# Performance work log

Hardware: AMD Instinct MI355X
Metric: run time of the kernel (lower is better)

The kernel has to match this reference:

```python
import jax, jax.numpy as jnp
import numpy as np

N_HEAD = 16
D_HEAD = 64
D_HIDN = 1024
B, S = 2, 2048
MASK_FILL = -1e9


def setup_inputs() -> dict:
    key = jax.random.key(0)
    ks = jax.random.split(key, 8)
    scale = 1.0 / np.sqrt(D_HIDN)
    return {
        "Q": jax.random.normal(ks[0], (B, S, D_HIDN), dtype=jnp.float32),
        "K": jax.random.normal(ks[1], (B, S, D_HIDN), dtype=jnp.float32),
        "V": jax.random.normal(ks[2], (B, S, D_HIDN), dtype=jnp.float32),
        "attn_mask": jnp.zeros((B, S, S), dtype=jnp.bool_),
        "Wq": jax.random.normal(ks[3], (D_HIDN, N_HEAD * D_HEAD), dtype=jnp.float32) * scale,
        "bq": jnp.zeros((N_HEAD * D_HEAD,), dtype=jnp.float32),
        "Wk": jax.random.normal(ks[4], (D_HIDN, N_HEAD * D_HEAD), dtype=jnp.float32) * scale,
        "bk": jnp.zeros((N_HEAD * D_HEAD,), dtype=jnp.float32),
        "Wv": jax.random.normal(ks[5], (D_HIDN, N_HEAD * D_HEAD), dtype=jnp.float32) * scale,
        "bv": jnp.zeros((N_HEAD * D_HEAD,), dtype=jnp.float32),
        "Wo": jax.random.normal(ks[6], (N_HEAD * D_HEAD, D_HIDN), dtype=jnp.float32) * scale,
        "bo": jnp.zeros((D_HIDN,), dtype=jnp.float32),
    }


def reference(Q, K, V, attn_mask, Wq, bq, Wk, bk, Wv, bv, Wo, bo):
    b, s, _ = Q.shape
    # projections -> [B, H, S, d_head]
    def split_heads(x):
        return x.reshape(b, -1, N_HEAD, D_HEAD).transpose(0, 2, 1, 3)
    q = split_heads(Q @ Wq + bq)
    k = split_heads(K @ Wk + bk)
    v = split_heads(V @ Wv + bv)
    # scaled dot-product attention with masked_fill(-1e9)
    scores = jnp.einsum("bhqd,bhkd->bhqk", q, k) / jnp.sqrt(jnp.float32(D_HEAD))
    scores = jnp.where(attn_mask[:, None, :, :], MASK_FILL, scores)
    attn_prob = jax.nn.softmax(scores, axis=-1)  # [B,H,S,S]
    context = jnp.einsum("bhqk,bhkd->bhqd", attn_prob, v)
    context = context.transpose(0, 2, 1, 3).reshape(b, s, N_HEAD * D_HEAD)
    output = context @ Wo + bo  # dropout is identity at eval
    return output, attn_prob
```

## Files before the change

### kernel.cpp

```cpp
#include <hip/hip_runtime.h>

typedef _Float16 f16;
typedef _Float16 f16x8 __attribute__((ext_vector_type(8)));
typedef _Float16 f16x4v __attribute__((ext_vector_type(4)));
typedef float f32x4 __attribute__((ext_vector_type(4)));

#define B_   2
#define S_   2048
#define H_   16
#define DH   64
#define DM   1024
#define BS_  (B_ * S_)

#if __has_builtin(__builtin_amdgcn_exp2f)
#define EXP2(x) __builtin_amdgcn_exp2f(x)
#else
#define EXP2(x) exp2f(x)
#endif

#define SCHED_FENCE() __builtin_amdgcn_sched_barrier(0)

__device__ __forceinline__ void gload16(const void* g, void* l) {
  __builtin_amdgcn_global_load_lds((const __attribute__((address_space(1))) unsigned int*)g,
                                   (__attribute__((address_space(3))) unsigned int*)l, 16, 0, 0);
}

__global__ __launch_bounds__(256) void cvt3(const float* __restrict__ a,
                                            const float* __restrict__ b,
                                            const float* __restrict__ c,
                                            f16* __restrict__ oa,
                                            f16* __restrict__ ob,
                                            f16* __restrict__ oc) {
  int t = blockIdx.y;
  const float* in = t == 0 ? a : (t == 1 ? b : c);
  f16* out = t == 0 ? oa : (t == 1 ? ob : oc);
  int i = (blockIdx.x * 256 + threadIdx.x) * 8;
  float4 x = *(const float4*)(in + i);
  float4 y = *(const float4*)(in + i + 4);
  f16x8 o;
  o[0] = (f16)x.x; o[1] = (f16)x.y; o[2] = (f16)x.z; o[3] = (f16)x.w;
  o[4] = (f16)y.x; o[5] = (f16)y.y; o[6] = (f16)y.z; o[7] = (f16)y.w;
  *(f16x8*)(out + i) = o;
}

__global__ __launch_bounds__(256) void wtrans4(const float* __restrict__ w0, const float* __restrict__ w1,
                                               const float* __restrict__ w2, const float* __restrict__ w3,
                                               f16* __restrict__ t0, f16* __restrict__ t1,
                                               f16* __restrict__ t2, f16* __restrict__ t3) {
  __shared__ float t[64][65];
  int z = blockIdx.z;
  const float* w = z == 0 ? w0 : (z == 1 ? w1 : (z == 2 ? w2 : w3));
  f16* wt = z == 0 ? t0 : (z == 1 ? t1 : (z == 2 ? t2 : t3));
  int r0 = blockIdx.y * 64, c0 = blockIdx.x * 64;
  int tid = threadIdx.x;
  int tr = tid >> 2, seg = tid & 3;
#pragma unroll
  for (int jj = 0; jj < 4; ++jj) {
    float4 v = *(const float4*)(w + (size_t)(r0 + tr) * DM + c0 + seg * 16 + jj * 4);
    t[tr][seg * 16 + jj * 4 + 0] = v.x;
    t[tr][seg * 16 + jj * 4 + 1] = v.y;
    t[tr][seg * 16 + jj * 4 + 2] = v.z;
    t[tr][seg * 16 + jj * 4 + 3] = v.w;
  }
  __syncthreads();
#pragma unroll
  for (int jj = 0; jj < 2; ++jj) {
    f16x8 o;
#pragma unroll
    for (int e = 0; e < 8; ++e) o[e] = (f16)t[seg * 16 + jj * 8 + e][tr];
    *(f16x8*)(wt + (size_t)(c0 + tr) * DM + r0 + seg * 16 + jj * 8) = o;
  }
}

__device__ __forceinline__ void gemm_core(const f16* __restrict__ A,
                                          const f16* __restrict__ Bt,
                                          int m0, int n0,
                                          char (&As)[2][16384], char (&Bs)[2][8192],
                                          f32x4 (&acc)[4][2]) {
  const int tid = threadIdx.x;
  const int lane = tid & 63, wid = tid >> 6;
  const int wr = wid >> 1, wc = wid & 1;
  const int l15 = lane & 15, l4 = lane >> 4;
#pragma unroll
  for (int mi = 0; mi < 4; ++mi)
#pragma unroll
    for (int ni = 0; ni < 2; ++ni) { acc[mi][ni][0]=0.f; acc[mi][ni][1]=0.f; acc[mi][ni][2]=0.f; acc[mi][ni][3]=0.f; }

  auto stage = [&](int buf, int kt) {
#pragma unroll
    for (int j = 0; j < 4; ++j) {
      int L = j * 256 + tid;
      int row = L >> 3, seg = L & 7;
      int so = (seg ^ (row & 7)) << 4;
      gload16((const char*)A + ((size_t)(m0 + row) * DM + kt) * 2 + so,
              As[buf] + j * 4096 + wid * 1024);
    }
#pragma unroll
    for (int j = 0; j < 2; ++j) {
      int L = j * 256 + tid;
      int row = L >> 3, seg = L & 7;
      int so = (seg ^ (row & 7)) << 4;
      gload16((const char*)Bt + ((size_t)(n0 + row) * DM + kt) * 2 + so,
              Bs[buf] + j * 4096 + wid * 1024);
    }
  };

  stage(0, 0);
  __syncthreads();
  for (int t = 0; t < 16; ++t) {
    int cur = t & 1;
    if (t < 15) stage(cur ^ 1, (t + 1) * 64);
#pragma unroll
    for (int kk = 0; kk < 2; ++kk) {
      f16x8 af[4], bf[2];
#pragma unroll
      for (int mi = 0; mi < 4; ++mi) {
        int row = wr * 64 + mi * 16 + l15;
        af[mi] = *(const f16x8*)(As[cur] + row * 128 + ((kk * 64 + l4 * 16) ^ ((row & 7) << 4)));
      }
#pragma unroll
      for (int ni = 0; ni < 2; ++ni) {
        int row = wc * 32 + ni * 16 + l15;
        bf[ni] = *(const f16x8*)(Bs[cur] + row * 128 + ((kk * 64 + l4 * 16) ^ ((row & 7) << 4)));
      }
#pragma unroll
      for (int mi = 0; mi < 4; ++mi)
#pragma unroll
        for (int ni = 0; ni < 2; ++ni)
          acc[mi][ni] = __builtin_amdgcn_mfma_f32_16x16x32_f16(af[mi], bf[ni], acc[mi][ni], 0, 0, 0);
    }
    __syncthreads();
  }
}

struct GemmPtrs { const f16* A; const f16* Bt; const float* bias; f16* outh; };

__global__ __launch_bounds__(256, 3) void gemm_proj(GemmPtrs p0, GemmPtrs p1, GemmPtrs p2,
                                                    f16* __restrict__ vout) {
  __shared__ __attribute__((aligned(16))) char As[2][16384];
  __shared__ __attribute__((aligned(16))) char Bs[2][8192];
  int lin = (blockIdx.z * 16 + blockIdx.y) * 32 + blockIdx.x;
  int swz = (lin & 7) * 192 + (lin >> 3);
  int z = swz >> 9, r = swz & 511;
  int m0 = (r >> 4) * 128, n0 = (r & 15) * 64;
  GemmPtrs g = z == 0 ? p0 : (z == 1 ? p1 : p2);

  f32x4 acc[4][2];
  gemm_core(g.A, g.Bt, m0, n0, As, Bs, acc);

  const int tid = threadIdx.x;
  const int lane = tid & 63, wid = tid >> 6;
  const int wr = wid >> 1, wc = wid & 1;
  const int l15 = lane & 15, l4 = lane >> 4;

  if (z != 2) {
#pragma unroll
    for (int mi = 0; mi < 4; ++mi)
#pragma unroll
      for (int ni = 0; ni < 2; ++ni) {
        int gcol = n0 + wc * 32 + ni * 16 + l15;
        float bv = g.bias[gcol];
#pragma unroll
        for (int rr = 0; rr < 4; ++rr) {
          int grow = m0 + wr * 64 + mi * 16 + l4 * 4 + rr;
          int b = grow >> 11, s = grow & 2047, h = gcol >> 6, d = gcol & 63;
          g.outh[(size_t)((b * H_ + h) * S_ + s) * DH + d] = (f16)(acc[mi][ni][rr] + bv);
        }
      }
  } else {
    f16* T2 = (f16*)&As[0][0];
#pragma unroll
    for (int mi = 0; mi < 4; ++mi)
#pragma unroll
      for (int ni = 0; ni < 2; ++ni) {
        int d = wc * 32 + ni * 16 + l15;
        int sl = wr * 64 + mi * 16 + l4 * 4;
        float bv = g.bias[n0 + d];
        f16x4v pv;
        pv[0] = (f16)(acc[mi][ni][0] + bv);
        pv[1] = (f16)(acc[mi][ni][1] + bv);
        pv[2] = (f16)(acc[mi][ni][2] + bv);
        pv[3] = (f16)(acc[mi][ni][3] + bv);
        *(f16x4v*)(T2 + d * 136 + sl) = pv;
      }
    __syncthreads();
    int d = tid >> 2, sq = tid & 3;
    int b = m0 >> 11, s0 = m0 & 2047, h = n0 >> 6;
    const f16* src = T2 + d * 136 + sq * 32;
    f16* dst = vout + ((size_t)((b * H_ + h) * DH + d)) * S_ + s0 + sq * 32;
#pragma unroll
    for (int j = 0; j < 4; ++j)
      *(f16x8*)(dst + j * 8) = *(const f16x8*)(src + j * 8);
  }
}

__global__ __launch_bounds__(256, 3) void gemm_out(const f16* __restrict__ A,
                                                   const f16* __restrict__ Bt,
                                                   const float* __restrict__ bias,
                                                   float* __restrict__ outf) {
  __shared__ __attribute__((aligned(16))) char As[2][16384];
  __shared__ __attribute__((aligned(16))) char Bs[2][8192];
  int lin = blockIdx.y * 32 + blockIdx.x;
  int swz = (lin & 7) * 64 + (lin >> 3);
  int m0 = (swz >> 4) * 128, n0 = (swz & 15) * 64;

  f32x4 acc[4][2];
  gemm_core(A, Bt, m0, n0, As, Bs, acc);

  const int tid = threadIdx.x;
  const int lane = tid & 63, wid = tid >> 6;
  const int wr = wid >> 1, wc = wid & 1;
  const int l15 = lane & 15, l4 = lane >> 4;
#pragma unroll
  for (int mi = 0; mi < 4; ++mi)
#pragma unroll
    for (int ni = 0; ni < 2; ++ni) {
      int gcol = n0 + wc * 32 + ni * 16 + l15;
      float bv = bias[gcol];
#pragma unroll
      for (int rr = 0; rr < 4; ++rr) {
        int grow = m0 + wr * 64 + mi * 16 + l4 * 4 + rr;
        outf[(size_t)grow * DM + gcol] = acc[mi][ni][rr] + bv;
      }
    }
}

__global__ __launch_bounds__(512, 4) void attn_kernel(const f16* __restrict__ q,
                                                      const f16* __restrict__ k,
                                                      const f16* __restrict__ vt,
                                                      const unsigned char* __restrict__ mask,
                                                      float* __restrict__ pout,
                                                      f16* __restrict__ ctxh) {
  __shared__ __attribute__((aligned(16))) char KV[4][8192];
  __shared__ __attribute__((aligned(16))) float P32[8][16][68];
  const int tid = threadIdx.x;
  const int lane = tid & 63, wid = tid >> 6;
  const int l15 = lane & 15, l4 = lane >> 4;

  int lin = blockIdx.y * 16 + blockIdx.x;
  int swz = (lin & 7) * 64 + (lin >> 3);
  const int bx = swz & 15, bh = swz >> 4;
  const int b = bh >> 4, h = bh & 15;
  const int q0w = bx * 128 + wid * 16;

  const f16* qb = q + (size_t)bh * S_ * DH;
  const char* kbc = (const char*)(k + (size_t)bh * S_ * DH);
  const char* vtbc = (const char*)(vt + (size_t)bh * DH * S_);
  const unsigned char* mb = mask + (size_t)b * S_ * S_;
  float* pb = pout + (size_t)bh * S_ * S_;

  const int srow = tid >> 3, sseg = tid & 7;
  const int soff = (sseg ^ (srow & 7)) << 4;

  auto stageK = [&](int buf, int t) {
    gload16(kbc + (size_t)(t * 64 + srow) * 128 + soff, KV[buf] + wid * 1024);
  };
  auto stageV = [&](int buf, int t) {
    gload16(vtbc + (size_t)srow * (S_ * 2) + (size_t)(t * 64) * 2 + soff, KV[buf] + wid * 1024);
  };

  unsigned mmask = 0;
  {
    const unsigned char* mrow = mb + (size_t)(q0w + (lane >> 2)) * S_ + (lane & 3) * 16;
    unsigned acc_or = 0;
#pragma unroll
    for (int tt = 0; tt < 4; ++tt) {
      uint4 mu[8];
#pragma unroll
      for (int u = 0; u < 8; ++u) mu[u] = *(const uint4*)(mrow + (tt * 8 + u) * 64);
#pragma unroll
      for (int u = 0; u < 8; ++u) acc_or |= mu[u].x | mu[u].y | mu[u].z | mu[u].w;
    }
    if (__any(acc_or != 0)) {
      for (int t = 0; t < 32; ++t) {
        uint4 mu = *(const uint4*)(mrow + t * 64);
        if (__any((mu.x | mu.y | mu.z | mu.w) != 0)) mmask |= 1u << t;
      }
    }
  }

  const f16 qs = (f16)0.18033688f;
  f16x8 aq[2];
#pragma unroll
  for (int hh = 0; hh < 2; ++hh) {
    f16x8 v = *(const f16x8*)(qb + (size_t)(q0w + l15) * DH + hh * 32 + l4 * 8);
#pragma unroll
    for (int j = 0; j < 8; ++j) v[j] = v[j] * qs;
    aq[hh] = v;
  }
  SCHED_FENCE();

  float sm[4] = {0.f, 0.f, 0.f, 0.f};

  stageK(0, 0);
  stageK(1, 1);
  for (int p = 0; p < 16; ++p) {
    asm volatile("s_waitcnt vmcnt(0)" ::: "memory");
    __builtin_amdgcn_s_barrier();
    SCHED_FENCE();
    if (p < 15) { stageK((2 * p + 2) & 3, 2 * p + 2); stageK((2 * p + 3) & 3, 2 * p + 3); }
    SCHED_FENCE();
#pragma unroll
    for (int u = 0; u < 2; ++u) {
      const int t = 2 * p + u;
      const char* Kb = KV[t & 3];
      const int kt = t * 64;
      const int anym = (mmask >> t) & 1;
#pragma unroll
      for (int f = 0; f < 4; ++f) {
        int krow = f * 16 + l15;
        f16x8 bk0 = *(const f16x8*)(Kb + krow * 128 + ((l4 * 16) ^ ((krow & 7) << 4)));
        f16x8 bk1 = *(const f16x8*)(Kb + krow * 128 + ((64 + l4 * 16) ^ ((krow & 7) << 4)));
        f32x4 s; s[0]=0.f; s[1]=0.f; s[2]=0.f; s[3]=0.f;
        __builtin_amdgcn_s_setprio(1);
        s = __builtin_amdgcn_mfma_f32_16x16x32_f16(aq[0], bk0, s, 0, 0, 0);
        s = __builtin_amdgcn_mfma_f32_16x16x32_f16(aq[1], bk1, s, 0, 0, 0);
        __builtin_amdgcn_s_setprio(0);
#pragma unroll
        for (int rr = 0; rr < 4; ++rr) {
          float sv = s[rr];
          if (anym) sv = mb[(size_t)(q0w + l4 * 4 + rr) * S_ + kt + f * 16 + l15] ? -1e9f : sv;
          sm[rr] += EXP2(sv);
        }
      }
    }
  }
#pragma unroll
  for (int d = 1; d < 16; d <<= 1)
#pragma unroll
    for (int rr = 0; rr < 4; ++rr) sm[rr] += __shfl_xor(sm[rr], d);
  float inv[4];
#pragma unroll
  for (int rr = 0; rr < 4; ++rr) inv[rr] = 1.0f / sm[rr];

  f32x4 ctx[4];
#pragma unroll
  for (int dc = 0; dc < 4; ++dc) { ctx[dc][0]=0.f; ctx[dc][1]=0.f; ctx[dc][2]=0.f; ctx[dc][3]=0.f; }

  __builtin_amdgcn_s_barrier();
  stageK(0, 0);
  stageV(2, 0);
  __syncthreads();
  for (int t = 0; t < 32; ++t) {
    const int cur = t & 1;
    const int kt = t * 64;
    if (t < 31) { stageK(cur ^ 1, t + 1); stageV(2 + (cur ^ 1), t + 1); }
    SCHED_FENCE();
    const int anym = (mmask >> t) & 1;

#pragma unroll
    for (int f = 0; f < 4; ++f) {
      int krow = f * 16 + l15;
      f16x8 bk0 = *(const f16x8*)(KV[cur] + krow * 128 + ((l4 * 16) ^ ((krow & 7) << 4)));
      f16x8 bk1 = *(const f16x8*)(KV[cur] + krow * 128 + ((64 + l4 * 16) ^ ((krow & 7) << 4)));
      f32x4 s; s[0]=0.f; s[1]=0.f; s[2]=0.f; s[3]=0.f;
      __builtin_amdgcn_s_setprio(1);
      s = __builtin_amdgcn_mfma_f32_16x16x32_f16(aq[0], bk0, s, 0, 0, 0);
      s = __builtin_amdgcn_mfma_f32_16x16x32_f16(aq[1], bk1, s, 0, 0, 0);
      __builtin_amdgcn_s_setprio(0);
#pragma unroll
      for (int rr = 0; rr < 4; ++rr) {
        float sv = s[rr];
        if (anym) sv = mb[(size_t)(q0w + l4 * 4 + rr) * S_ + kt + f * 16 + l15] ? -1e9f : sv;
        float p = EXP2(sv) * inv[rr];
        P32[wid][l4 * 4 + rr][f * 16 + l15] = p;
      }
    }
#pragma unroll
    for (int j = 0; j < 4; ++j) {
      int row = j * 4 + l4;
      f32x4 v = *(const f32x4*)&P32[wid][row][l15 * 4];
      __builtin_nontemporal_store(v, (f32x4*)(pb + (size_t)(q0w + row) * S_ + kt + l15 * 4));
    }
#pragma unroll
    for (int kk = 0; kk < 2; ++kk) {
      f32x4 x = *(const f32x4*)&P32[wid][l15][kk * 32 + l4 * 8];
      f32x4 y = *(const f32x4*)&P32[wid][l15][kk * 32 + l4 * 8 + 4];
      f16x8 pa;
      pa[0] = (f16)x[0]; pa[1] = (f16)x[1]; pa[2] = (f16)x[2]; pa[3] = (f16)x[3];
      pa[4] = (f16)y[0]; pa[5] = (f16)y[1]; pa[6] = (f16)y[2]; pa[7] = (f16)y[3];
      f16x8 bv0, bv1, bv2, bv3;
      {
        int vr0 = 0 * 16 + l15, vr1 = 1 * 16 + l15, vr2 = 2 * 16 + l15, vr3 = 3 * 16 + l15;
        bv0 = *(const f16x8*)(KV[2 + cur] + vr0 * 128 + ((kk * 64 + l4 * 16) ^ ((vr0 & 7) << 4)));
        bv1 = *(const f16x8*)(KV[2 + cur] + vr1 * 128 + ((kk * 64 + l4 * 16) ^ ((vr1 & 7) << 4)));
        bv2 = *(const f16x8*)(KV[2 + cur] + vr2 * 128 + ((kk * 64 + l4 * 16) ^ ((vr2 & 7) << 4)));
        bv3 = *(const f16x8*)(KV[2 + cur] + vr3 * 128 + ((kk * 64 + l4 * 16) ^ ((vr3 & 7) << 4)));
      }
      __builtin_amdgcn_s_setprio(1);
      ctx[0] = __builtin_amdgcn_mfma_f32_16x16x32_f16(pa, bv0, ctx[0], 0, 0, 0);
      ctx[1] = __builtin_amdgcn_mfma_f32_16x16x32_f16(pa, bv1, ctx[1], 0, 0, 0);
      ctx[2] = __builtin_amdgcn_mfma_f32_16x16x32_f16(pa, bv2, ctx[2], 0, 0, 0);
      ctx[3] = __builtin_amdgcn_mfma_f32_16x16x32_f16(pa, bv3, ctx[3], 0, 0, 0);
      __builtin_amdgcn_s_setprio(0);
    }

    if (t < 31) {
      asm volatile("s_waitcnt vmcnt(4)" ::: "memory");
      __builtin_amdgcn_s_barrier();
      SCHED_FENCE();
    }
  }

#pragma unroll
  for (int dc = 0; dc < 4; ++dc)
#pragma unroll
    for (int rr = 0; rr < 4; ++rr)
      ctxh[(size_t)(b * S_ + q0w + l4 * 4 + rr) * DM + h * DH + dc * 16 + l15] = (f16)ctx[dc][rr];
}

extern "C" void kernel_launch(void* const* d_in, const int* in_sizes, int n_in,
                              void* d_out, int out_size, void* d_ws, size_t ws_size,
                              hipStream_t stream) {
  (void)in_sizes; (void)n_in; (void)out_size; (void)ws_size;
  const float* Q  = (const float*)d_in[0];
  const float* K  = (const float*)d_in[1];
  const float* V  = (const float*)d_in[2];
  const unsigned char* mask = (const unsigned char*)d_in[3];
  const float* Wq = (const float*)d_in[4];
  const float* bq = (const float*)d_in[5];
  const float* Wk = (const float*)d_in[6];
  const float* bk = (const float*)d_in[7];
  const float* Wv = (const float*)d_in[8];
  const float* bv = (const float*)d_in[9];
  const float* Wo = (const float*)d_in[10];
  const float* bo = (const float*)d_in[11];

  f16* ws = (f16*)d_ws;
  f16* Xq  = ws;
  f16* Xk  = Xq + 4194304;
  f16* Xv  = Xk + 4194304;
  f16* Wqt = Xv + 4194304;
  f16* Wkt = Wqt + 1048576;
  f16* Wvt = Wkt + 1048576;
  f16* Wot = Wvt + 1048576;
  f16* qh  = Wot + 1048576;
  f16* kh  = qh + 4194304;
  f16* vth = kh + 4194304;
  f16* ctx = Xq;

  float* out0 = (float*)d_out;
  float* pout = out0 + (size_t)BS_ * DM;

  cvt3<<<dim3(2048, 3), dim3(256), 0, stream>>>(Q, K, V, Xq, Xk, Xv);
  wtrans4<<<dim3(16, 16, 4), dim3(256), 0, stream>>>(Wq, Wk, Wv, Wo, Wqt, Wkt, Wvt, Wot);

  GemmPtrs pq{Xq, Wqt, bq, qh};
  GemmPtrs pk{Xk, Wkt, bk, kh};
  GemmPtrs pv{Xv, Wvt, bv, nullptr};
  gemm_proj<<<dim3(32, 16, 3), dim3(256), 0, stream>>>(pq, pk, pv, vth);

  attn_kernel<<<dim3(16, 32), dim3(512), 0, stream>>>(qh, kh, vth, mask, pout, ctx);

  gemm_out<<<dim3(32, 16), dim3(256), 0, stream>>>(ctx, Wot, bo, out0);
}
```

Baseline: 229.7 us.

## Merge input prep kernels and enlarge GEMM tiles to 128x128 with 512 threads

Fuses the fp16 conversion and weight-transpose kernels into one launch, saving a kernel launch and the gap between them. The projection and output GEMMs move from 128x64 tiles with 4 waves to 128x128 tiles with 8 waves. This halves the block count and raises reuse of the A operand, at the cost of more LDS per block and lower occupancy for gemm_out. The V-transpose epilogue now handles two heads per block in two LDS passes.

```diff
diff --git a/kernel.cpp b/kernel.cpp
--- a/kernel.cpp
+++ b/kernel.cpp
@@ -25,61 +25,61 @@
                                    (__attribute__((address_space(3))) unsigned int*)l, 16, 0, 0);
 }
 
-__global__ __launch_bounds__(256) void cvt3(const float* __restrict__ a,
-                                            const float* __restrict__ b,
-                                            const float* __restrict__ c,
-                                            f16* __restrict__ oa,
-                                            f16* __restrict__ ob,
-                                            f16* __restrict__ oc) {
-  int t = blockIdx.y;
-  const float* in = t == 0 ? a : (t == 1 ? b : c);
-  f16* out = t == 0 ? oa : (t == 1 ? ob : oc);
-  int i = (blockIdx.x * 256 + threadIdx.x) * 8;
-  float4 x = *(const float4*)(in + i);
-  float4 y = *(const float4*)(in + i + 4);
-  f16x8 o;
-  o[0] = (f16)x.x; o[1] = (f16)x.y; o[2] = (f16)x.z; o[3] = (f16)x.w;
-  o[4] = (f16)y.x; o[5] = (f16)y.y; o[6] = (f16)y.z; o[7] = (f16)y.w;
-  *(f16x8*)(out + i) = o;
-}
-
-__global__ __launch_bounds__(256) void wtrans4(const float* __restrict__ w0, const float* __restrict__ w1,
-                                               const float* __restrict__ w2, const float* __restrict__ w3,
-                                               f16* __restrict__ t0, f16* __restrict__ t1,
-                                               f16* __restrict__ t2, f16* __restrict__ t3) {
-  __shared__ float t[64][65];
-  int z = blockIdx.z;
-  const float* w = z == 0 ? w0 : (z == 1 ? w1 : (z == 2 ? w2 : w3));
-  f16* wt = z == 0 ? t0 : (z == 1 ? t1 : (z == 2 ? t2 : t3));
-  int r0 = blockIdx.y * 64, c0 = blockIdx.x * 64;
+__global__ __launch_bounds__(256) void prep(const float* __restrict__ Q, const float* __restrict__ K,
+                                            const float* __restrict__ V,
+                                            f16* __restrict__ Xq, f16* __restrict__ Xk, f16* __restrict__ Xv,
+                                            const float* __restrict__ w0, const float* __restrict__ w1,
+                                            const float* __restrict__ w2, const float* __restrict__ w3,
+                                            f16* __restrict__ t0, f16* __restrict__ t1,
+                                            f16* __restrict__ t2, f16* __restrict__ t3) {
+  int bid = blockIdx.x;
   int tid = threadIdx.x;
-  int tr = tid >> 2, seg = tid & 3;
-#pragma unroll
-  for (int jj = 0; jj < 4; ++jj) {
-    float4 v = *(const float4*)(w + (size_t)(r0 + tr) * DM + c0 + seg * 16 + jj * 4);
-    t[tr][seg * 16 + jj * 4 + 0] = v.x;
-    t[tr][seg * 16 + jj * 4 + 1] = v.y;
-    t[tr][seg * 16 + jj * 4 + 2] = v.z;
-    t[tr][seg * 16 + jj * 4 + 3] = v.w;
-  }
-  __syncthreads();
-#pragma unroll
-  for (int jj = 0; jj < 2; ++jj) {
+  if (bid < 6144) {
+    int t = bid >> 11;
+    const float* in = t == 0 ? Q : (t == 1 ? K : V);
+    f16* out = t == 0 ? Xq : (t == 1 ? Xk : Xv);
+    int i = ((bid & 2047) * 256 + tid) * 8;
+    float4 x = *(const float4*)(in + i);
+    float4 y = *(const float4*)(in + i + 4);
     f16x8 o;
-#pragma unroll
-    for (int e = 0; e < 8; ++e) o[e] = (f16)t[seg * 16 + jj * 8 + e][tr];
-    *(f16x8*)(wt + (size_t)(c0 + tr) * DM + r0 + seg * 16 + jj * 8) = o;
+    o[0] = (f16)x.x; o[1] = (f16)x.y; o[2] = (f16)x.z; o[3] = (f16)x.w;
+    o[4] = (f16)y.x; o[5] = (f16)y.y; o[6] = (f16)y.z; o[7] = (f16)y.w;
+    *(f16x8*)(out + i) = o;
+  } else {
+    __shared__ float t[64][65];
+    int w = bid - 6144;
+    int z = w >> 8, rr = w & 255;
+    const float* wsrc = z == 0 ? w0 : (z == 1 ? w1 : (z == 2 ? w2 : w3));
+    f16* wt = z == 0 ? t0 : (z == 1 ? t1 : (z == 2 ? t2 : t3));
+    int r0 = (rr >> 4) * 64, c0 = (rr & 15) * 64;
+    int tr = tid >> 2, seg = tid & 3;
+#pragma unroll
+    for (int jj = 0; jj < 4; ++jj) {
+      float4 v = *(const float4*)(wsrc + (size_t)(r0 + tr) * DM + c0 + seg * 16 + jj * 4);
+      t[tr][seg * 16 + jj * 4 + 0] = v.x;
+      t[tr][seg * 16 + jj * 4 + 1] = v.y;
+      t[tr][seg * 16 + jj * 4 + 2] = v.z;
+      t[tr][seg * 16 + jj * 4 + 3] = v.w;
+    }
+    __syncthreads();
+#pragma unroll
+    for (int jj = 0; jj < 2; ++jj) {
+      f16x8 o;
+#pragma unroll
+      for (int e = 0; e < 8; ++e) o[e] = (f16)t[seg * 16 + jj * 8 + e][tr];
+      *(f16x8*)(wt + (size_t)(c0 + tr) * DM + r0 + seg * 16 + jj * 8) = o;
+    }
   }
 }
 
 __device__ __forceinline__ void gemm_core(const f16* __restrict__ A,
                                           const f16* __restrict__ Bt,
                                           int m0, int n0,
-                                          char (&As)[2][16384], char (&Bs)[2][8192],
+                                          char (&As)[2][16384], char (&Bs)[2][16384],
                                           f32x4 (&acc)[4][2]) {
   const int tid = threadIdx.x;
   const int lane = tid & 63, wid = tid >> 6;
-  const int wr = wid >> 1, wc = wid & 1;
+  const int wr = wid >> 2, wc = wid & 3;
   const int l15 = lane & 15, l4 = lane >> 4;
 #pragma unroll
   for (int mi = 0; mi < 4; ++mi)
@@ -88,20 +88,14 @@
 
   auto stage = [&](int buf, int kt) {
 #pragma unroll
-    for (int j = 0; j < 4; ++j) {
-      int L = j * 256 + tid;
+    for (int j = 0; j < 2; ++j) {
+      int L = j * 512 + tid;
       int row = L >> 3, seg = L & 7;
       int so = (seg ^ (row & 7)) << 4;
       gload16((const char*)A + ((size_t)(m0 + row) * DM + kt) * 2 + so,
-              As[buf] + j * 4096 + wid * 1024);
-    }
-#pragma unroll
-    for (int j = 0; j < 2; ++j) {
-      int L = j * 256 + tid;
-      int row = L >> 3, seg = L & 7;
-      int so = (seg ^ (row & 7)) << 4;
+              As[buf] + j * 8192 + wid * 1024);
       gload16((const char*)Bt + ((size_t)(n0 + row) * DM + kt) * 2 + so,
-              Bs[buf] + j * 4096 + wid * 1024);
+              Bs[buf] + j * 8192 + wid * 1024);
     }
   };
 
@@ -135,14 +129,14 @@
 
 struct GemmPtrs { const f16* A; const f16* Bt; const float* bias; f16* outh; };
 
-__global__ __launch_bounds__(256, 3) void gemm_proj(GemmPtrs p0, GemmPtrs p1, GemmPtrs p2,
+__global__ __launch_bounds__(512, 4) void gemm_proj(GemmPtrs p0, GemmPtrs p1, GemmPtrs p2,
                                                     f16* __restrict__ vout) {
   __shared__ __attribute__((aligned(16))) char As[2][16384];
-  __shared__ __attribute__((aligned(16))) char Bs[2][8192];
-  int lin = (blockIdx.z * 16 + blockIdx.y) * 32 + blockIdx.x;
-  int swz = (lin & 7) * 192 + (lin >> 3);
-  int z = swz >> 9, r = swz & 511;
-  int m0 = (r >> 4) * 128, n0 = (r & 15) * 64;
+  __shared__ __attribute__((aligned(16))) char Bs[2][16384];
+  int lin = (blockIdx.z * 8 + blockIdx.y) * 32 + blockIdx.x;
+  int swz = (lin & 7) * 96 + (lin >> 3);
+  int z = swz >> 8, r = swz & 255;
+  int m0 = (r >> 3) * 128, n0 = (r & 7) * 128;
   GemmPtrs g = z == 0 ? p0 : (z == 1 ? p1 : p2);
 
   f32x4 acc[4][2];
@@ -150,7 +144,7 @@
 
   const int tid = threadIdx.x;
   const int lane = tid & 63, wid = tid >> 6;
-  const int wr = wid >> 1, wc = wid & 1;
+  const int wr = wid >> 2, wc = wid & 3;
   const int l15 = lane & 15, l4 = lane >> 4;
 
   if (z != 2) {
@@ -169,47 +163,56 @@
       }
   } else {
     f16* T2 = (f16*)&As[0][0];
-#pragma unroll
-    for (int mi = 0; mi < 4; ++mi)
-#pragma unroll
-      for (int ni = 0; ni < 2; ++ni) {
-        int d = wc * 32 + ni * 16 + l15;
-        int sl = wr * 64 + mi * 16 + l4 * 4;
-        float bv = g.bias[n0 + d];
-        f16x4v pv;
-        pv[0] = (f16)(acc[mi][ni][0] + bv);
-        pv[1] = (f16)(acc[mi][ni][1] + bv);
-        pv[2] = (f16)(acc[mi][ni][2] + bv);
-        pv[3] = (f16)(acc[mi][ni][3] + bv);
-        *(f16x4v*)(T2 + d * 136 + sl) = pv;
-      }
-    __syncthreads();
-    int d = tid >> 2, sq = tid & 3;
-    int b = m0 >> 11, s0 = m0 & 2047, h = n0 >> 6;
-    const f16* src = T2 + d * 136 + sq * 32;
-    f16* dst = vout + ((size_t)((b * H_ + h) * DH + d)) * S_ + s0 + sq * 32;
-#pragma unroll
-    for (int j = 0; j < 4; ++j)
-      *(f16x8*)(dst + j * 8) = *(const f16x8*)(src + j * 8);
-  }
-}
-
-__global__ __launch_bounds__(256, 3) void gemm_out(const f16* __restrict__ A,
+    int b = m0 >> 11, s0 = m0 & 2047;
+#pragma unroll
+    for (int hh = 0; hh < 2; ++hh) {
+      if ((wc >> 1) == hh) {
+        int dl = (wc & 1) * 32;
+#pragma unroll
+        for (int mi = 0; mi < 4; ++mi)
+#pragma unroll
+          for (int ni = 0; ni < 2; ++ni) {
+            int d = dl + ni * 16 + l15;
+            int sl = wr * 64 + mi * 16 + l4 * 4;
+            float bv = g.bias[n0 + hh * 64 + d];
+            f16x4v pv;
+            pv[0] = (f16)(acc[mi][ni][0] + bv);
+            pv[1] = (f16)(acc[mi][ni][1] + bv);
+            pv[2] = (f16)(acc[mi][ni][2] + bv);
+            pv[3] = (f16)(acc[mi][ni][3] + bv);
+            *(f16x4v*)(T2 + d * 136 + sl) = pv;
+          }
+      }
+      __syncthreads();
+      {
+        int d = tid >> 3, sq = tid & 7;
+        int head = (n0 >> 6) + hh;
+        const f16* src = T2 + d * 136 + sq * 16;
+        f16* dst = vout + ((size_t)((b * H_ + head) * DH + d)) * S_ + s0 + sq * 16;
+        *(f16x8*)(dst)     = *(const f16x8*)(src);
+        *(f16x8*)(dst + 8) = *(const f16x8*)(src + 8);
+      }
+      if (hh == 0) __syncthreads();
+    }
+  }
+}
+
+__global__ __launch_bounds__(512, 2) void gemm_out(const f16* __restrict__ A,
                                                    const f16* __restrict__ Bt,
                                                    const float* __restrict__ bias,
                                                    float* __restrict__ outf) {
   __shared__ __attribute__((aligned(16))) char As[2][16384];
-  __shared__ __attribute__((aligned(16))) char Bs[2][8192];
+  __shared__ __attribute__((aligned(16))) char Bs[2][16384];
   int lin = blockIdx.y * 32 + blockIdx.x;
-  int swz = (lin & 7) * 64 + (lin >> 3);
-  int m0 = (swz >> 4) * 128, n0 = (swz & 15) * 64;
+  int swz = (lin & 7) * 32 + (lin >> 3);
+  int m0 = (swz >> 3) * 128, n0 = (swz & 7) * 128;
 
   f32x4 acc[4][2];
   gemm_core(A, Bt, m0, n0, As, Bs, acc);
 
   const int tid = threadIdx.x;
   const int lane = tid & 63, wid = tid >> 6;
-  const int wr = wid >> 1, wc = wid & 1;
+  const int wr = wid >> 2, wc = wid & 3;
   const int l15 = lane & 15, l4 = lane >> 4;
 #pragma unroll
   for (int mi = 0; mi < 4; ++mi)
@@ -442,15 +445,15 @@
   float* out0 = (float*)d_out;
   float* pout = out0 + (size_t)BS_ * DM;
 
-  cvt3<<<dim3(2048, 3), dim3(256), 0, stream>>>(Q, K, V, Xq, Xk, Xv);
-  wtrans4<<<dim3(16, 16, 4), dim3(256), 0, stream>>>(Wq, Wk, Wv, Wo, Wqt, Wkt, Wvt, Wot);
+  prep<<<dim3(7168), dim3(256), 0, stream>>>(Q, K, V, Xq, Xk, Xv,
+                                             Wq, Wk, Wv, Wo, Wqt, Wkt, Wvt, Wot);
 
   GemmPtrs pq{Xq, Wqt, bq, qh};
   GemmPtrs pk{Xk, Wkt, bk, kh};
   GemmPtrs pv{Xv, Wvt, bv, nullptr};
-  gemm_proj<<<dim3(32, 16, 3), dim3(256), 0, stream>>>(pq, pk, pv, vth);
+  gemm_proj<<<dim3(32, 8, 3), dim3(512), 0, stream>>>(pq, pk, pv, vth);
 
   attn_kernel<<<dim3(16, 32), dim3(512), 0, stream>>>(qh, kh, vth, mask, pout, ctx);
 
-  gemm_out<<<dim3(32, 16), dim3(256), 0, stream>>>(ctx, Wot, bo, out0);
-}
+  gemm_out<<<dim3(32, 8), dim3(512), 0, stream>>>(ctx, Wot, bo, out0);
+}
```

Result: faster. 224.2 us, median of 2 (-2.4%).
